# Performance work log

Measured on AMD Instinct MI355X. Metric: run time of the kernel, lower is better.

## Reference

```python
import jax, jax.numpy as jnp
import numpy as np

B, N, F_IN, F_OUT, K = 4, 8192, 32, 64, 4


def setup_inputs() -> dict:
    key = jax.random.key(0)
    k0, k1, k2, k3 = jax.random.split(key, 4)
    x = jax.random.normal(k0, (B, N, F_IN), dtype=jnp.float32)
    # dense rescaled-Laplacian-like symmetric operator, spectrally ~O(1)
    A = jax.random.normal(k1, (N, N), dtype=jnp.float32) / np.float32(np.sqrt(N))
    L = 0.5 * (A + A.T)
    stdv = np.float32(1.0 / np.sqrt(F_IN * K))  # matches uniform(in_channels*K, .)
    weight = jax.random.uniform(k2, (K, F_IN, F_OUT), dtype=jnp.float32, minval=-stdv, maxval=stdv)
    bias = jax.random.uniform(k3, (1, N, F_OUT), dtype=jnp.float32, minval=-stdv, maxval=stdv)
    return {"x": x, "L": L, "weight": weight, "bias": bias}


def _chebyshev(L, x, K):
    # Faithful to the torch code: X is overwritten by L @ X each step (matrix
    # powers), and Xt[k] = 2 * L^k x - Xt[k-2]. This is NOT the textbook
    # Chebyshev recurrence, but it is what the module computes.
    Xt = [x]
    X = x
    if K > 1:
        X = jnp.einsum('ab,cbe->cae', L, X)  # [B,N,F]
        Xt.append(X)
    for k in range(2, K):
        X = jnp.einsum('ab,cbe->cae', L, X)
        Xt.append(2.0 * X - Xt[k - 2])
    return jnp.stack(Xt)  # [K,B,N,F]


def reference(x, L, weight, bias):
    Kdim = weight.shape[0]
    xc = _chebyshev(L, x, Kdim)                       # [K,B,N,F]
    out = jnp.einsum('abcd,ade->bce', xc, weight)     # contract K and F_in
    return out + bias                                 # [B,N,F_out]
```

## Files before the change

kernel.cpp:

```cpp
#include <hip/hip_runtime.h>


typedef __bf16 bf16;
typedef bf16 bf16x8 __attribute__((ext_vector_type(8)));
typedef bf16 bf16x4 __attribute__((ext_vector_type(4)));
typedef float f32x4 __attribute__((ext_vector_type(4)));

static_assert(sizeof(bf16x8) == 16, "bf16x8 must be 16B");

#define N_DIM 8192
#define NCOLS 128
#define BM 128
#define BK 32
#define SPLITS 8
#define KCHUNK (N_DIM / SPLITS)
#define LDS_STRIDE 40

__device__ inline unsigned short f2bf_bits(float f) {
    bf16 b = (bf16)f;
    return __builtin_bit_cast(unsigned short, b);
}

__global__ __launch_bounds__(256) void pack_x_kernel(
    const float* __restrict__ x, bf16* __restrict__ Xb0) {
    int g = blockIdx.x * 256 + threadIdx.x;
    int n = g & 8191;
    int c = g >> 13;
    int b = c >> 5, fi = c & 31;
    Xb0[(size_t)c * N_DIM + n] = (bf16)x[((size_t)b * N_DIM + n) * 32 + fi];
}

__global__ __launch_bounds__(256) void init_out_kernel(
    const float* __restrict__ x, const float* __restrict__ w,
    const float* __restrict__ bias, float* __restrict__ out) {
    __shared__ float weff0[32 * 64];
    __shared__ float xs[16 * 32];
    int t = threadIdx.x;
    for (int i = t; i < 2048; i += 256) weff0[i] = w[i] - w[2 * 2048 + i];
    int r0 = blockIdx.x * 16;
    for (int i = t; i < 512; i += 256) {
        int lr = i >> 5, fi = i & 31;
        xs[i] = x[(size_t)(r0 + lr) * 32 + fi];
    }
    __syncthreads();
    for (int i = t; i < 1024; i += 256) {
        int lr = i >> 6, fo = i & 63;
        int r = r0 + lr;
        float acc = bias[(size_t)(r & 8191) * 64 + fo];
#pragma unroll
        for (int fi = 0; fi < 32; fi++)
            acc += xs[lr * 32 + fi] * weff0[fi * 64 + fo];
        out[(size_t)r * 64 + fo] = acc;
    }
}

__global__ __launch_bounds__(256, 2) void gemm_kernel(
    const float* __restrict__ L, const bf16* __restrict__ Xb,
    float* __restrict__ part) {
    __shared__ bf16 As[BM * LDS_STRIDE];
    __shared__ bf16 Bs[NCOLS * LDS_STRIDE];

    const int mt = blockIdx.x;
    const int sp = blockIdx.y;
    const int rbase = mt * BM;
    const int kbase = sp * KCHUNK;
    const int t = threadIdx.x;
    const int lane = t & 63;
    const int wave = t >> 6;
    const int wr = wave >> 1, wc = wave & 1;
    const int lm = lane & 15, kq = lane >> 4;

    f32x4 acc[4][4];
    const f32x4 zero = {0.f, 0.f, 0.f, 0.f};
#pragma unroll
    for (int mi = 0; mi < 4; mi++)
#pragma unroll
        for (int ni = 0; ni < 4; ni++) acc[mi][ni] = zero;

    const int arow = t >> 3;
    const int ac4 = t & 7;

    for (int kk = 0; kk < KCHUNK; kk += BK) {
#pragma unroll
        for (int i = 0; i < 4; i++) {
            int row = arow + i * 32;
            const float4 v = *(const float4*)(
                &L[(size_t)(rbase + row) * N_DIM + kbase + kk + ac4 * 4]);
            bf16x4 p;
            p[0] = (bf16)v.x; p[1] = (bf16)v.y; p[2] = (bf16)v.z; p[3] = (bf16)v.w;
            *(bf16x4*)(&As[row * LDS_STRIDE + ac4 * 4]) = p;
        }
#pragma unroll
        for (int j = 0; j < 2; j++) {
            int id = t + 256 * j;
            int col = id >> 2, jj = id & 3;
            const uint4 v = *(const uint4*)(
                &Xb[(size_t)col * N_DIM + kbase + kk + jj * 8]);
            *(uint4*)(&Bs[col * LDS_STRIDE + jj * 8]) = v;
        }
        __syncthreads();

        bf16x8 af[4], bfr[4];
#pragma unroll
        for (int i = 0; i < 4; i++)
            af[i] = *(const bf16x8*)(&As[(wr * 64 + i * 16 + lm) * LDS_STRIDE + kq * 8]);
#pragma unroll
        for (int i = 0; i < 4; i++)
            bfr[i] = *(const bf16x8*)(&Bs[(wc * 64 + i * 16 + lm) * LDS_STRIDE + kq * 8]);
#pragma unroll
        for (int mi = 0; mi < 4; mi++)
#pragma unroll
            for (int ni = 0; ni < 4; ni++)
                acc[mi][ni] = __builtin_amdgcn_mfma_f32_16x16x32_bf16(
                    af[mi], bfr[ni], acc[mi][ni], 0, 0, 0);
        __syncthreads();
    }

    float* P = part + (size_t)sp * N_DIM * NCOLS;
#pragma unroll
    for (int mi = 0; mi < 4; mi++) {
        int row0 = rbase + wr * 64 + mi * 16 + kq * 4;
#pragma unroll
        for (int ni = 0; ni < 4; ni++) {
            int col = wc * 64 + ni * 16 + lm;
#pragma unroll
            for (int r = 0; r < 4; r++)
                P[(size_t)(row0 + r) * NCOLS + col] = acc[mi][ni][r];
        }
    }
}

__global__ __launch_bounds__(256) void combine_kernel(
    const float* __restrict__ part, const float* __restrict__ w,
    float* __restrict__ out, bf16* __restrict__ XbNext, int pass) {
    __shared__ float Yt[128 * 66];
    __shared__ float weff[32 * 64];
    int t = threadIdx.x;
    int n0 = blockIdx.x * 64;

    for (int i = t; i < 2048; i += 256) {
        float v;
        if (pass == 1)      v = w[1 * 2048 + i] - w[3 * 2048 + i];
        else if (pass == 2) v = 2.f * w[2 * 2048 + i];
        else                v = 2.f * w[3 * 2048 + i];
        weff[i] = v;
    }
    for (int slot = t; slot < 2048; slot += 256) {
        int row = slot >> 5;
        int c4 = slot & 31;
        float4 s = {0.f, 0.f, 0.f, 0.f};
#pragma unroll
        for (int sp = 0; sp < SPLITS; sp++) {
            const float4 v = *(const float4*)(
                &part[(size_t)sp * N_DIM * NCOLS + (size_t)(n0 + row) * NCOLS + c4 * 4]);
            s.x += v.x; s.y += v.y; s.z += v.z; s.w += v.w;
        }
        Yt[(c4 * 4 + 0) * 66 + row] = s.x;
        Yt[(c4 * 4 + 1) * 66 + row] = s.y;
        Yt[(c4 * 4 + 2) * 66 + row] = s.z;
        Yt[(c4 * 4 + 3) * 66 + row] = s.w;
    }
    __syncthreads();
    if (pass < 3) {
        int c = t >> 1;
        int nh = (t & 1) * 32;
#pragma unroll
        for (int v4 = 0; v4 < 4; v4++) {
            union { uint4 u; unsigned short s[8]; } pk;
#pragma unroll
            for (int j = 0; j < 8; j++)
                pk.s[j] = f2bf_bits(Yt[c * 66 + nh + v4 * 8 + j]);
            *(uint4*)(&XbNext[(size_t)c * N_DIM + n0 + nh + v4 * 8]) = pk.u;
        }
    }
    int b = t >> 6, fo = t & 63;
    for (int n = 0; n < 64; n++) {
        size_t oidx = ((size_t)b * N_DIM + n0 + n) * 64 + fo;
        float accv = out[oidx];
#pragma unroll
        for (int fi = 0; fi < 32; fi++)
            accv += Yt[(b * 32 + fi) * 66 + n] * weff[fi * 64 + fo];
        out[oidx] = accv;
    }
}

extern "C" void kernel_launch(void* const* d_in, const int* in_sizes, int n_in,
                              void* d_out, int out_size, void* d_ws, size_t ws_size,
                              hipStream_t stream) {
    const float* x    = (const float*)d_in[0];
    const float* L    = (const float*)d_in[1];
    const float* w    = (const float*)d_in[2];
    const float* bias = (const float*)d_in[3];
    float* out = (float*)d_out;

    char* ws = (char*)d_ws;
    bf16* XbA  = (bf16*)ws;
    bf16* XbB  = (bf16*)(ws + (2ull << 20));
    float* part = (float*)(ws + (4ull << 20));

    pack_x_kernel<<<(NCOLS * N_DIM) / 256, 256, 0, stream>>>(x, XbA);
    init_out_kernel<<<(4 * N_DIM) / 16, 256, 0, stream>>>(x, w, bias, out);

    dim3 ggrid(N_DIM / BM, SPLITS);
    gemm_kernel<<<ggrid, 256, 0, stream>>>(L, XbA, part);
    combine_kernel<<<N_DIM / 64, 256, 0, stream>>>(part, w, out, XbB, 1);
    gemm_kernel<<<ggrid, 256, 0, stream>>>(L, XbB, part);
    combine_kernel<<<N_DIM / 64, 256, 0, stream>>>(part, w, out, XbA, 2);
    gemm_kernel<<<ggrid, 256, 0, stream>>>(L, XbA, part);
    combine_kernel<<<N_DIM / 64, 256, 0, stream>>>(part, w, out, XbA, 3);
}
```

Before: 654.9 us.

## Pre-convert L to bf16 once and stream tiles via direct global-to-LDS loads

Adds a kernel that converts the fp32 L matrix to bf16 once per call, so the three GEMM passes each read half the bytes instead of fp32 L. The GEMM now loads L and X tiles with global_load_lds into an XOR-swizzled LDS layout, bypassing registers, and doubles BK to 64 with two MFMA sub-steps per tile. The conversion pass costs an extra full read of fp32 L plus a write of the 128MB bf16 copy. The swizzle is meant to avoid LDS bank conflicts without padding.

```diff
diff --git a/kernel.cpp b/kernel.cpp
--- a/kernel.cpp
+++ b/kernel.cpp
@@ -11,14 +11,28 @@
 #define N_DIM 8192
 #define NCOLS 128
 #define BM 128
-#define BK 32
+#define BK 64
 #define SPLITS 8
 #define KCHUNK (N_DIM / SPLITS)
-#define LDS_STRIDE 40
 
 __device__ inline unsigned short f2bf_bits(float f) {
     bf16 b = (bf16)f;
     return __builtin_bit_cast(unsigned short, b);
+}
+
+__device__ inline void load_lds16(const bf16* g, bf16* l) {
+    __builtin_amdgcn_global_load_lds(
+        (const __attribute__((address_space(1))) void*)g,
+        (__attribute__((address_space(3))) void*)l, 16, 0, 0);
+}
+
+__global__ __launch_bounds__(256) void convert_L_kernel(
+    const float* __restrict__ L, bf16* __restrict__ Lb) {
+    size_t i = ((size_t)blockIdx.x * 256 + threadIdx.x) * 4;
+    const float4 v = *(const float4*)(L + i);
+    bf16x4 p;
+    p[0] = (bf16)v.x; p[1] = (bf16)v.y; p[2] = (bf16)v.z; p[3] = (bf16)v.w;
+    *(bf16x4*)(Lb + i) = p;
 }
 
 __global__ __launch_bounds__(256) void pack_x_kernel(
@@ -55,21 +69,24 @@
 }
 
 __global__ __launch_bounds__(256, 2) void gemm_kernel(
-    const float* __restrict__ L, const bf16* __restrict__ Xb,
+    const bf16* __restrict__ Lb, const bf16* __restrict__ Xb,
     float* __restrict__ part) {
-    __shared__ bf16 As[BM * LDS_STRIDE];
-    __shared__ bf16 Bs[NCOLS * LDS_STRIDE];
+    __shared__ bf16 As[BM * BK];
+    __shared__ bf16 Bs[NCOLS * BK];
 
     const int mt = blockIdx.x;
     const int sp = blockIdx.y;
     const int rbase = mt * BM;
-    const int kbase = sp * KCHUNK;
+    const size_t kbase = (size_t)sp * KCHUNK;
     const int t = threadIdx.x;
     const int lane = t & 63;
     const int wave = t >> 6;
     const int wr = wave >> 1, wc = wave & 1;
     const int lm = lane & 15, kq = lane >> 4;
 
+    const int lrow = lane >> 3;
+    const int jb = (lane & 7) ^ lrow;
+
     f32x4 acc[4][4];
     const f32x4 zero = {0.f, 0.f, 0.f, 0.f};
 #pragma unroll
@@ -77,42 +94,40 @@
 #pragma unroll
         for (int ni = 0; ni < 4; ni++) acc[mi][ni] = zero;
 
-    const int arow = t >> 3;
-    const int ac4 = t & 7;
-
     for (int kk = 0; kk < KCHUNK; kk += BK) {
 #pragma unroll
         for (int i = 0; i < 4; i++) {
-            int row = arow + i * 32;
-            const float4 v = *(const float4*)(
-                &L[(size_t)(rbase + row) * N_DIM + kbase + kk + ac4 * 4]);
-            bf16x4 p;
-            p[0] = (bf16)v.x; p[1] = (bf16)v.y; p[2] = (bf16)v.z; p[3] = (bf16)v.w;
-            *(bf16x4*)(&As[row * LDS_STRIDE + ac4 * 4]) = p;
-        }
-#pragma unroll
-        for (int j = 0; j < 2; j++) {
-            int id = t + 256 * j;
-            int col = id >> 2, jj = id & 3;
-            const uint4 v = *(const uint4*)(
-                &Xb[(size_t)col * N_DIM + kbase + kk + jj * 8]);
-            *(uint4*)(&Bs[col * LDS_STRIDE + jj * 8]) = v;
+            const int c = wave * 4 + i;
+            const int row = 8 * c + lrow;
+            load_lds16(&Lb[(size_t)(rbase + row) * N_DIM + kbase + kk + jb * 8],
+                       &As[c * 512]);
+            load_lds16(&Xb[(size_t)row * N_DIM + kbase + kk + jb * 8],
+                       &Bs[c * 512]);
         }
         __syncthreads();
 
-        bf16x8 af[4], bfr[4];
-#pragma unroll
-        for (int i = 0; i < 4; i++)
-            af[i] = *(const bf16x8*)(&As[(wr * 64 + i * 16 + lm) * LDS_STRIDE + kq * 8]);
-#pragma unroll
-        for (int i = 0; i < 4; i++)
-            bfr[i] = *(const bf16x8*)(&Bs[(wc * 64 + i * 16 + lm) * LDS_STRIDE + kq * 8]);
-#pragma unroll
-        for (int mi = 0; mi < 4; mi++)
-#pragma unroll
-            for (int ni = 0; ni < 4; ni++)
-                acc[mi][ni] = __builtin_amdgcn_mfma_f32_16x16x32_bf16(
-                    af[mi], bfr[ni], acc[mi][ni], 0, 0, 0);
+#pragma unroll
+        for (int ks = 0; ks < 2; ks++) {
+            bf16x8 af[4], bfr[4];
+#pragma unroll
+            for (int mi = 0; mi < 4; mi++) {
+                int r = wr * 64 + mi * 16 + lm;
+                int cb = (kq + 4 * ks) ^ (lm & 7);
+                af[mi] = *(const bf16x8*)(&As[r * BK + cb * 8]);
+            }
+#pragma unroll
+            for (int ni = 0; ni < 4; ni++) {
+                int r = wc * 64 + ni * 16 + lm;
+                int cb = (kq + 4 * ks) ^ (lm & 7);
+                bfr[ni] = *(const bf16x8*)(&Bs[r * BK + cb * 8]);
+            }
+#pragma unroll
+            for (int mi = 0; mi < 4; mi++)
+#pragma unroll
+                for (int ni = 0; ni < 4; ni++)
+                    acc[mi][ni] = __builtin_amdgcn_mfma_f32_16x16x32_bf16(
+                        af[mi], bfr[ni], acc[mi][ni], 0, 0, 0);
+        }
         __syncthreads();
     }
 
@@ -194,18 +209,20 @@
     float* out = (float*)d_out;
 
     char* ws = (char*)d_ws;
-    bf16* XbA  = (bf16*)ws;
-    bf16* XbB  = (bf16*)(ws + (2ull << 20));
-    float* part = (float*)(ws + (4ull << 20));
-
+    bf16* Lb   = (bf16*)ws;
+    bf16* XbA  = (bf16*)(ws + (128ull << 20));
+    bf16* XbB  = (bf16*)(ws + (130ull << 20));
+    float* part = (float*)(ws + (132ull << 20));
+
+    convert_L_kernel<<<(N_DIM * (size_t)N_DIM) / (4 * 256), 256, 0, stream>>>(L, Lb);
     pack_x_kernel<<<(NCOLS * N_DIM) / 256, 256, 0, stream>>>(x, XbA);
     init_out_kernel<<<(4 * N_DIM) / 16, 256, 0, stream>>>(x, w, bias, out);
 
     dim3 ggrid(N_DIM / BM, SPLITS);
-    gemm_kernel<<<ggrid, 256, 0, stream>>>(L, XbA, part);
+    gemm_kernel<<<ggrid, 256, 0, stream>>>(Lb, XbA, part);
     combine_kernel<<<N_DIM / 64, 256, 0, stream>>>(part, w, out, XbB, 1);
-    gemm_kernel<<<ggrid, 256, 0, stream>>>(L, XbB, part);
+    gemm_kernel<<<ggrid, 256, 0, stream>>>(Lb, XbB, part);
     combine_kernel<<<N_DIM / 64, 256, 0, stream>>>(part, w, out, XbA, 2);
-    gemm_kernel<<<ggrid, 256, 0, stream>>>(L, XbA, part);
+    gemm_kernel<<<ggrid, 256, 0, stream>>>(Lb, XbA, part);
     combine_kernel<<<N_DIM / 64, 256, 0, stream>>>(part, w, out, XbA, 3);
 }
```

Measured after the change: 545.1 us. 16.8% less time.
